# Kernel optimization log

Measured on AMD Instinct MI355X. Metric: run time of the kernel, lower is better.

Reference implementation:

```python
import jax, jax.numpy as jnp
import numpy as np

B, N, S, K, D = 8, 16384, 1024, 32, 64
MLP = [64, 64, 128]
C_IN = 3 + D  # grouped_xyz_norm (3) concat grouped point features (D)
EPS = 1e-5


def setup_inputs() -> dict:
    key = jax.random.key(0)
    ks = jax.random.split(key, 16)
    inp = {
        "xyz": jax.random.normal(ks[0], (B, 3, N), dtype=jnp.float32),
        "points": jax.random.normal(ks[1], (B, D, N), dtype=jnp.float32),
        "sample_idx": jax.random.randint(ks[2], (B, S), 0, N, dtype=jnp.int32),
    }
    last = C_IN
    for i, oc in enumerate(MLP):
        scale = 1.0 / np.sqrt(last)
        inp[f"w{i}"] = jax.random.uniform(ks[3 + 4 * i], (oc, last), jnp.float32, -scale, scale)
        inp[f"b{i}"] = jax.random.uniform(ks[4 + 4 * i], (oc,), jnp.float32, -scale, scale)
        inp[f"g{i}"] = jnp.ones((oc,), jnp.float32)   # BN gamma
        inp[f"be{i}"] = jnp.zeros((oc,), jnp.float32)  # BN beta
        last = oc
    return inp


def _gather(pts, idx):
    # pts: [B,N,C], idx: [B,...] -> [B,...,C]
    return jax.vmap(lambda p, i: p[i])(pts, idx)


def _mlp_layer(x, w, b, g, be):
    # x: [B,C,K,S]; 1x1 Conv2d + BatchNorm2d (training-mode batch stats) + ReLU
    y = jnp.einsum("bcks,oc->boks", x, w) + b[None, :, None, None]
    mu = jnp.mean(y, axis=(0, 2, 3), keepdims=True)
    var = jnp.var(y, axis=(0, 2, 3), keepdims=True)
    y = (y - mu) * jax.lax.rsqrt(var + EPS)
    y = y * g[None, :, None, None] + be[None, :, None, None]
    return jax.nn.relu(y)


def reference(xyz, points, sample_idx, w0, b0, g0, be0, w1, b1, g1, be1, w2, b2, g2, be2):
    xyz_t = jnp.transpose(xyz, (0, 2, 1))      # [B,N,3]
    pts_t = jnp.transpose(points, (0, 2, 1))   # [B,N,D]
    idx_s = sample_idx.astype(jnp.int32)

    new_xyz = _gather(xyz_t, idx_s)            # [B,S,3]

    # square_distance(new_xyz, xyz): [B,S,N]
    d = (jnp.sum(new_xyz ** 2, -1)[:, :, None]
         + jnp.sum(xyz_t ** 2, -1)[:, None, :]
         - 2.0 * jnp.einsum("bsc,bnc->bsn", new_xyz, xyz_t))
    _, idx = jax.lax.top_k(-d, K)              # kNN indices [B,S,K]

    grouped_xyz = _gather(xyz_t, idx)          # [B,S,K,3]
    grouped_norm = grouped_xyz - new_xyz[:, :, None, :]
    grouped_pts = _gather(pts_t, idx)          # [B,S,K,D]
    feat = jnp.concatenate([grouped_norm, grouped_pts], axis=-1)  # [B,S,K,3+D]

    x = jnp.transpose(feat, (0, 3, 2, 1))      # [B,C,K,S]
    x = _mlp_layer(x, w0, b0, g0, be0)
    x = _mlp_layer(x, w1, b1, g1, be1)
    x = _mlp_layer(x, w2, b2, g2, be2)
    new_points = jnp.max(x, axis=2)            # [B,128,S]

    return (jnp.transpose(new_xyz, (0, 2, 1)), new_points, grouped_xyz, idx_s)
```

## Files before the change

### kernel.cpp

```cpp
#include <hip/hip_runtime.h>

constexpr int cB = 8, cN = 16384, cS = 1024, cK = 32, cD = 64;
constexpr int cO2 = 128;
constexpr int PTOT = cB * cS * cK;
constexpr int NBLK = PTOT / 64;
constexpr int C2POS = 128;
constexpr int NBLK2 = PTOT / C2POS;

constexpr int OUT1_OFF = cB * 3 * cS;
constexpr int OUT2_OFF = OUT1_OFF + cB * cO2 * cS;
constexpr int OUT3_OFF = OUT2_OFF + cB * cS * cK * 3;

constexpr size_t WS_PTS  = 0;
constexpr size_t WS_XYZP = WS_PTS  + (size_t)cB * cN * cD * 4;
constexpr size_t WS_IDX  = WS_XYZP + (size_t)cB * cN * 16;
constexpr size_t WS_NORM = WS_IDX  + (size_t)PTOT * 4;
constexpr size_t WS_Y0   = WS_NORM + (size_t)PTOT * 3 * 4;
constexpr size_t WS_Y1   = WS_Y0   + (size_t)PTOT * 64 * 4;
constexpr size_t WS_MX   = WS_Y1   + (size_t)PTOT * 64 * 4;
constexpr size_t WS_MN   = WS_MX   + (size_t)cB * cS * cO2 * 4;
constexpr size_t WS_P0   = WS_MN   + (size_t)cB * cS * cO2 * 4;
constexpr size_t WS_P1   = WS_P0   + (size_t)NBLK * 64 * 2 * 8;
constexpr size_t WS_P2   = WS_P1   + (size_t)NBLK * 64 * 2 * 8;
constexpr size_t WS_BN   = WS_P2   + (size_t)NBLK * 128 * 2 * 8;
constexpr size_t WS_END  = WS_BN   + 3 * 128 * 2 * 4;

__device__ __forceinline__ unsigned keyOf(float d) {
    unsigned u = __float_as_uint(d);
    return u ^ ((unsigned)((int)u >> 31) | 0x80000000u);
}
__device__ __forceinline__ float distNp(float qx, float qy, float qz, float sq, float4 p) {
    float m0 = __fmul_rn(qx, p.x);
    float m1 = __fmul_rn(qy, p.y);
    float m2 = __fmul_rn(qz, p.z);
    float dt = __fadd_rn(__fadd_rn(m0, m1), m2);
    return __fsub_rn(__fadd_rn(sq, p.w), __fmul_rn(2.0f, dt));
}

__global__ __launch_bounds__(256) void k_pack(const float* __restrict__ xyz,
                                              float4* __restrict__ xyzp) {
    int i = blockIdx.x * 256 + threadIdx.x;
    int b = i >> 14, n = i & (cN - 1);
    float x = xyz[(b * 3 + 0) * cN + n];
    float y = xyz[(b * 3 + 1) * cN + n];
    float z = xyz[(b * 3 + 2) * cN + n];
    float sq = __fadd_rn(__fadd_rn(__fmul_rn(x, x), __fmul_rn(y, y)), __fmul_rn(z, z));
    xyzp[i] = make_float4(x, y, z, sq);
}

__global__ __launch_bounds__(256) void k_tr(const float* __restrict__ pts,
                                            float* __restrict__ ptsT) {
    __shared__ float tile[64][65];
    int b = blockIdx.y;
    int n0 = blockIdx.x * 64;
    int tid = threadIdx.x;
    for (int it = 0; it < 16; ++it) {
        int l = it * 256 + tid;
        int c = l >> 6, nn = l & 63;
        tile[nn][c] = pts[((size_t)b * 64 + c) * cN + n0 + nn];
    }
    __syncthreads();
    for (int it = 0; it < 16; ++it) {
        int l = it * 256 + tid;
        int nn = l >> 6, c = l & 63;
        ptsT[((size_t)(b * cN + n0 + nn)) * 64 + c] = tile[nn][c];
    }
}

#define QB 8
#define CAPU 896
#define CAP2 192

__device__ __forceinline__ void selectBin2(const unsigned* __restrict__ h, int lane,
                                           int target, int* Tout, int* cbOut) {
    int base = lane * 8;
    unsigned hh[8];
    unsigned c8 = 0;
#pragma unroll
    for (int i = 0; i < 8; i++) { hh[i] = h[base + i]; c8 += hh[i]; }
    unsigned incl = c8;
#pragma unroll
    for (int off = 1; off < 32; off <<= 1) {
        unsigned t = __shfl_up(incl, (unsigned)off, 32);
        if (lane >= off) incl += t;
    }
    int excl = (int)(incl - c8);
    if (excl < target && target <= (int)incl) {
        int c = excl;
#pragma unroll
        for (int i = 0; i < 8; i++) {
            int nc = c + (int)hh[i];
            if (c < target && target <= nc) { *Tout = base + i; *cbOut = c; }
            c = nc;
        }
    }
}

__global__ __launch_bounds__(256, 4) void k_knn(const float* __restrict__ xyz,
                                                const int* __restrict__ sidx_g,
                                                const float4* __restrict__ xyzp,
                                                int* __restrict__ idxw,
                                                float* __restrict__ normw,
                                                float* __restrict__ outbuf) {
    __shared__ unsigned hist[QB][258];
    __shared__ unsigned short candU[QB][CAPU];
    __shared__ unsigned long long cand2[QB][CAP2];
    __shared__ unsigned cnt[QB], cnt2[QB];
    __shared__ float qxs[QB], qys[QB], qzs[QB], sqs[QB];
    __shared__ int sIdx[QB];
    __shared__ float s1s[QB], tAs[QB], tBs[QB];
    __shared__ int T1s[QB], cb1s[QB], T2s[QB], cb2s[QB];
    __shared__ float fTs[QB];
    __shared__ int ovf[QB], nRf[QB];
    __shared__ int anyR, anyOvfR, anyOvfC;
    __shared__ unsigned order[QB][cK];

    int tid = threadIdx.x;
    int qi = tid >> 5, lane = tid & 31;
    int qbase = blockIdx.x * QB;
    int b = qbase / cS;
    int s0 = qbase % cS;
    const float4* pb = xyzp + (size_t)b * cN;

    if (tid < QB) {
        int si = sidx_g[b * cS + s0 + tid];
        sIdx[tid] = si;
        float x = xyz[(b * 3 + 0) * cN + si];
        float y = xyz[(b * 3 + 1) * cN + si];
        float z = xyz[(b * 3 + 2) * cN + si];
        qxs[tid] = x; qys[tid] = y; qzs[tid] = z;
        sqs[tid] = __fadd_rn(__fadd_rn(__fmul_rn(x, x), __fmul_rn(y, y)), __fmul_rn(z, z));
        cnt[tid] = 0u; cnt2[tid] = 0u;
    }
    if (tid == 0) { anyR = 0; anyOvfR = 0; anyOvfC = 0; }
    for (int i = tid; i < QB * 258; i += 256) ((unsigned*)hist)[i] = 0u;
    __syncthreads();

    float qx = qxs[qi], qy = qys[qi], qz = qzs[qi], qsq = sqs[qi];

    {
        float dmin = 3.4e38f;
        for (int t = 0; t < 64; ++t) {
            float4 p = pb[lane + 32 * t];
            float dot = fmaf(qx, p.x, fmaf(qy, p.y, qz * p.z));
            float d = fmaf(-2.0f, dot, qsq + p.w);
            dmin = fminf(dmin, d);
        }
        float rmax = dmin;
#pragma unroll
        for (int off = 16; off; off >>= 1)
            rmax = fmaxf(rmax, __shfl_xor(rmax, off, 32));
        if (lane == 0) {
            float R = fmaxf(rmax, 1e-12f);
            float s1 = 254.0f / R;
            s1s[qi] = s1;
            tAs[qi] = qsq * s1;
            tBs[qi] = -2.0f * s1;
        }
    }
    __syncthreads();

    float lqx[QB], lqy[QB], lqz[QB], lS[QB], lA[QB], lB[QB];
#pragma unroll
    for (int q = 0; q < QB; q++) {
        lqx[q] = qxs[q]; lqy[q] = qys[q]; lqz[q] = qzs[q];
        lS[q] = s1s[q]; lA[q] = tAs[q]; lB[q] = tBs[q];
    }

    for (int j = 0; j < cN / 256; ++j) {
        int n = j * 256 + tid;
        float4 p = pb[n];
#pragma unroll
        for (int q = 0; q < QB; ++q) {
            float dot = fmaf(lqx[q], p.x, fmaf(lqy[q], p.y, lqz[q] * p.z));
            float t = fmaf(dot, lB[q], fmaf(p.w, lS[q], lA[q]));
            if (t < 258.0f) {
                int bin = __float2int_rz(fmaxf(t, 0.0f));
                atomicAdd(&hist[q][bin], 1u);
                unsigned pos = atomicAdd(&cnt[q], 1u);
                if (pos < CAPU) candU[q][pos] = (unsigned short)n;
            }
        }
    }
    __syncthreads();

    selectBin2(hist[qi], lane, cK, &T1s[qi], &cb1s[qi]);
    __syncthreads();
    if (tid < QB) {
        int T1 = T1s[tid];
        int acc = cb1s[tid] + (int)hist[tid][T1] + (int)hist[tid][T1 + 1];
        int ov = (cnt[tid] > CAPU) ? 1 : 0;
        int nr = (acc > CAP2) ? 1 : 0;
        ovf[tid] = ov; nRf[tid] = nr;
        fTs[tid] = (float)(T1 + 2);
        if (nr) atomicOr(&anyR, 1);
        if (nr && ov) atomicOr(&anyOvfR, 1);
        if (ov) atomicOr(&anyOvfC, 1);
    }
    __syncthreads();

    if (anyR) {
        for (int i = tid; i < QB * 258; i += 256) ((unsigned*)hist)[i] = 0u;
        __syncthreads();
        if (anyOvfR) {
            int lT1[QB], go[QB];
#pragma unroll
            for (int q = 0; q < QB; q++) { lT1[q] = T1s[q]; go[q] = nRf[q] & ovf[q]; }
            for (int j = 0; j < cN / 256; ++j) {
                float4 p = pb[j * 256 + tid];
#pragma unroll
                for (int q = 0; q < QB; ++q) {
                    if (go[q]) {
                        float dot = fmaf(lqx[q], p.x, fmaf(lqy[q], p.y, lqz[q] * p.z));
                        float t = fmaf(dot, lB[q], fmaf(p.w, lS[q], lA[q]));
                        float um = fmaxf(t, 0.0f) - (float)lT1[q];
                        if (um >= 0.0f && um < 2.0f)
                            atomicAdd(&hist[q][min(255, __float2int_rz(um * 128.0f))], 1u);
                    }
                }
            }
        }
        if (nRf[qi] && !ovf[qi]) {
            float fT1 = (float)T1s[qi];
            int m = (int)cnt[qi];
            for (int i = lane; i < m; i += 32) {
                int n = candU[qi][i];
                float4 p = pb[n];
                float dot = fmaf(qx, p.x, fmaf(qy, p.y, qz * p.z));
                float t = fmaf(dot, tBs[qi], fmaf(p.w, s1s[qi], tAs[qi]));
                float um = fmaxf(t, 0.0f) - fT1;
                if (um >= 0.0f && um < 2.0f)
                    atomicAdd(&hist[qi][min(255, __float2int_rz(um * 128.0f))], 1u);
            }
        }
        __syncthreads();
        if (nRf[qi]) selectBin2(hist[qi], lane, cK - cb1s[qi], &T2s[qi], &cb2s[qi]);
        __syncthreads();
        if (tid < QB && nRf[tid])
            fTs[tid] = (float)T1s[tid] + (float)(T2s[tid] + 2) * 0.0078125f;
        __syncthreads();
    }

    if (anyOvfC) {
        float lt[QB]; int go[QB]; float lsq[QB];
#pragma unroll
        for (int q = 0; q < QB; q++) { lt[q] = fTs[q]; go[q] = ovf[q]; lsq[q] = sqs[q]; }
        for (int j = 0; j < cN / 256; ++j) {
            int n = j * 256 + tid;
            float4 p = pb[n];
#pragma unroll
            for (int q = 0; q < QB; ++q) {
                if (go[q]) {
                    float dot = fmaf(lqx[q], p.x, fmaf(lqy[q], p.y, lqz[q] * p.z));
                    float t = fmaf(dot, lB[q], fmaf(p.w, lS[q], lA[q]));
                    if (t < lt[q]) {
                        float de = distNp(lqx[q], lqy[q], lqz[q], lsq[q], p);
                        unsigned pos = atomicAdd(&cnt2[q], 1u);
                        if (pos < CAP2)
                            cand2[q][pos] = ((unsigned long long)keyOf(de) << 32) | (unsigned)n;
                    }
                }
            }
        }
    }
    if (!ovf[qi]) {
        float fT = fTs[qi];
        int m = (int)cnt[qi];
        for (int i = lane; i < m; i += 32) {
            int n = candU[qi][i];
            float4 p = pb[n];
            float dot = fmaf(qx, p.x, fmaf(qy, p.y, qz * p.z));
            float t = fmaf(dot, tBs[qi], fmaf(p.w, s1s[qi], tAs[qi]));
            if (t < fT) {
                float de = distNp(qx, qy, qz, qsq, p);
                unsigned pos = atomicAdd(&cnt2[qi], 1u);
                if (pos < CAP2)
                    cand2[qi][pos] = ((unsigned long long)keyOf(de) << 32) | (unsigned)n;
            }
        }
    }
    __syncthreads();

    int m2 = (int)min(cnt2[qi], (unsigned)CAP2);
    for (int r = 0; r < cK; ++r) {
        unsigned long long best = ~0ull;
        int bslot = -1;
        for (int i = lane; i < m2; i += 32) {
            unsigned long long v = cand2[qi][i];
            if (v < best) { best = v; bslot = i; }
        }
#pragma unroll
        for (int off = 16; off; off >>= 1) {
            unsigned long long ov = __shfl_xor(best, off, 32);
            int os = __shfl_xor(bslot, off, 32);
            if (ov < best) { best = ov; bslot = os; }
        }
        if (lane == 0) {
            order[qi][r] = (best != ~0ull) ? (unsigned)(best & 0xFFFFFFFFull) : 0u;
            if (bslot >= 0) cand2[qi][bslot] = ~0ull;
        }
    }

    {
        int r = lane;
        int s = s0 + qi;
        int n = (int)order[qi][r];
        size_t pos = (size_t)(b * cS + s) * cK + r;
        idxw[pos] = n;
        float px = xyz[(b * 3 + 0) * cN + n];
        float py = xyz[(b * 3 + 1) * cN + n];
        float pz = xyz[(b * 3 + 2) * cN + n];
        outbuf[OUT2_OFF + pos * 3 + 0] = px;
        outbuf[OUT2_OFF + pos * 3 + 1] = py;
        outbuf[OUT2_OFF + pos * 3 + 2] = pz;
        normw[pos * 3 + 0] = __fsub_rn(px, qxs[qi]);
        normw[pos * 3 + 1] = __fsub_rn(py, qys[qi]);
        normw[pos * 3 + 2] = __fsub_rn(pz, qzs[qi]);
        if (r == 0) {
            outbuf[OUT3_OFF + b * cS + s] = (float)sIdx[qi];
            outbuf[(b * 3 + 0) * cS + s] = qxs[qi];
            outbuf[(b * 3 + 1) * cS + s] = qys[qi];
            outbuf[(b * 3 + 2) * cS + s] = qzs[qi];
        }
    }
}

__global__ __launch_bounds__(256) void k_conv0(const int* __restrict__ idxw,
                                               const float* __restrict__ normw,
                                               const float* __restrict__ ptsT,
                                               const float* __restrict__ w0,
                                               const float* __restrict__ b0,
                                               float* __restrict__ y0,
                                               double* __restrict__ part0) {
    __shared__ __align__(16) float fA[64][68];
    __shared__ __align__(16) float wT[68 * 68];
    __shared__ float ps[16][64];
    __shared__ float pq[16][64];
    __shared__ float bl[64];
    int tid = threadIdx.x;
    int blk = blockIdx.x;
    int b = blk >> 9;
    int s0 = (blk & 511) << 1;
    size_t posbase = ((size_t)b * cS + s0) * cK;

    for (int l = tid; l < 64 * 67; l += 256) {
        int o = l / 67, c = l - o * 67;
        wT[c * 68 + o] = w0[l];
    }
    if (tid < 68) wT[67 * 68 + tid] = 0.0f;
    if (tid < 64) bl[tid] = b0[tid];
    {
        int kk = tid >> 2, p = tid & 3;
        size_t pos = posbase + kk;
        int n = idxw[pos];
        const float* pr = ptsT + ((size_t)b * cN + n) * 64 + p * 16;
        float* frow = &fA[kk][3 + p * 16];
#pragma unroll
        for (int q4 = 0; q4 < 4; q4++) {
            float4 v = *(const float4*)(pr + q4 * 4);
            frow[q4 * 4 + 0] = v.x; frow[q4 * 4 + 1] = v.y;
            frow[q4 * 4 + 2] = v.z; frow[q4 * 4 + 3] = v.w;
        }
        if (p == 0) {
            fA[kk][0] = normw[pos * 3 + 0];
            fA[kk][1] = normw[pos * 3 + 1];
            fA[kk][2] = normw[pos * 3 + 2];
            fA[kk][67] = 0.0f;
        }
    }
    __syncthreads();

    int ty = tid >> 4, tx = tid & 15;
    float acc[4][4];
#pragma unroll
    for (int i = 0; i < 4; i++)
#pragma unroll
        for (int j = 0; j < 4; j++) acc[i][j] = bl[tx * 4 + j];

    for (int c4 = 0; c4 < 17; ++c4) {
        float4 wv[4];
#pragma unroll
        for (int cc = 0; cc < 4; cc++)
            wv[cc] = *(const float4*)&wT[(c4 * 4 + cc) * 68 + tx * 4];
#pragma unroll
        for (int i = 0; i < 4; i++) {
            float4 a = *(const float4*)&fA[ty * 4 + i][c4 * 4];
            acc[i][0] = fmaf(a.x, wv[0].x, acc[i][0]);
            acc[i][1] = fmaf(a.x, wv[0].y, acc[i][1]);
            acc[i][2] = fmaf(a.x, wv[0].z, acc[i][2]);
            acc[i][3] = fmaf(a.x, wv[0].w, acc[i][3]);
            acc[i][0] = fmaf(a.y, wv[1].x, acc[i][0]);
            acc[i][1] = fmaf(a.y, wv[1].y, acc[i][1]);
            acc[i][2] = fmaf(a.y, wv[1].z, acc[i][2]);
            acc[i][3] = fmaf(a.y, wv[1].w, acc[i][3]);
            acc[i][0] = fmaf(a.z, wv[2].x, acc[i][0]);
            acc[i][1] = fmaf(a.z, wv[2].y, acc[i][1]);
            acc[i][2] = fmaf(a.z, wv[2].z, acc[i][2]);
            acc[i][3] = fmaf(a.z, wv[2].w, acc[i][3]);
            acc[i][0] = fmaf(a.w, wv[3].x, acc[i][0]);
            acc[i][1] = fmaf(a.w, wv[3].y, acc[i][1]);
            acc[i][2] = fmaf(a.w, wv[3].z, acc[i][2]);
            acc[i][3] = fmaf(a.w, wv[3].w, acc[i][3]);
        }
    }
#pragma unroll
    for (int i = 0; i < 4; i++) {
        int kk = ty * 4 + i;
        float4 o4 = make_float4(acc[i][0], acc[i][1], acc[i][2], acc[i][3]);
        *(float4*)(y0 + (posbase + kk) * 64 + tx * 4) = o4;
    }
#pragma unroll
    for (int j = 0; j < 4; j++) {
        float s = acc[0][j] + acc[1][j] + acc[2][j] + acc[3][j];
        float q = acc[0][j] * acc[0][j] + acc[1][j] * acc[1][j] +
                  acc[2][j] * acc[2][j] + acc[3][j] * acc[3][j];
        ps[ty][tx * 4 + j] = s;
        pq[ty][tx * 4 + j] = q;
    }
    __syncthreads();
    if (tid < 64) {
        float s = 0.f, q = 0.f;
        for (int t = 0; t < 16; t++) { s += ps[t][tid]; q += pq[t][tid]; }
        part0[((size_t)blk * 64 + tid) * 2 + 0] = (double)s;
        part0[((size_t)blk * 64 + tid) * 2 + 1] = (double)q;
    }
}

__global__ __launch_bounds__(256) void k_conv1(const float* __restrict__ yin,
                                               const float2* __restrict__ bnin,
                                               const float* __restrict__ w,
                                               const float* __restrict__ bb,
                                               float* __restrict__ yout,
                                               double* __restrict__ part) {
    __shared__ __align__(16) float fA[64][68];
    __shared__ __align__(16) float wT[64 * 68];
    __shared__ float ps[16][64];
    __shared__ float pq[16][64];
    __shared__ float bl[64], al[64], sl[64];
    int tid = threadIdx.x;
    int blk = blockIdx.x;
    int b = blk >> 9;
    int s0 = (blk & 511) << 1;
    size_t posbase = ((size_t)b * cS + s0) * cK;

    if (tid < 64) {
        bl[tid] = bb[tid];
        float2 t = bnin[tid];
        al[tid] = t.x; sl[tid] = t.y;
    }
    __syncthreads();
    for (int l = tid; l < 64 * 64; l += 256) {
        int o = l >> 6, c = l & 63;
        wT[c * 68 + o] = w[l];
    }
    {
        int kk = tid >> 2, p = tid & 3;
        const float* yr = yin + (posbase + kk) * 64 + p * 16;
#pragma unroll
        for (int q4 = 0; q4 < 4; q4++) {
            float4 v = *(const float4*)(yr + q4 * 4);
            int c = p * 16 + q4 * 4;
            v.x = fmaxf(fmaf(v.x, al[c + 0], sl[c + 0]), 0.0f);
            v.y = fmaxf(fmaf(v.y, al[c + 1], sl[c + 1]), 0.0f);
            v.z = fmaxf(fmaf(v.z, al[c + 2], sl[c + 2]), 0.0f);
            v.w = fmaxf(fmaf(v.w, al[c + 3], sl[c + 3]), 0.0f);
            *(float4*)&fA[kk][c] = v;
        }
    }
    __syncthreads();

    int ty = tid >> 4, tx = tid & 15;
    float acc[4][4];
#pragma unroll
    for (int i = 0; i < 4; i++)
#pragma unroll
        for (int j = 0; j < 4; j++) acc[i][j] = bl[tx * 4 + j];

    for (int c4 = 0; c4 < 16; ++c4) {
        float4 wv[4];
#pragma unroll
        for (int cc = 0; cc < 4; cc++)
            wv[cc] = *(const float4*)&wT[(c4 * 4 + cc) * 68 + tx * 4];
#pragma unroll
        for (int i = 0; i < 4; i++) {
            float4 a = *(const float4*)&fA[ty * 4 + i][c4 * 4];
            acc[i][0] = fmaf(a.x, wv[0].x, acc[i][0]);
            acc[i][1] = fmaf(a.x, wv[0].y, acc[i][1]);
            acc[i][2] = fmaf(a.x, wv[0].z, acc[i][2]);
            acc[i][3] = fmaf(a.x, wv[0].w, acc[i][3]);
            acc[i][0] = fmaf(a.y, wv[1].x, acc[i][0]);
            acc[i][1] = fmaf(a.y, wv[1].y, acc[i][1]);
            acc[i][2] = fmaf(a.y, wv[1].z, acc[i][2]);
            acc[i][3] = fmaf(a.y, wv[1].w, acc[i][3]);
            acc[i][0] = fmaf(a.z, wv[2].x, acc[i][0]);
            acc[i][1] = fmaf(a.z, wv[2].y, acc[i][1]);
            acc[i][2] = fmaf(a.z, wv[2].z, acc[i][2]);
            acc[i][3] = fmaf(a.z, wv[2].w, acc[i][3]);
            acc[i][0] = fmaf(a.w, wv[3].x, acc[i][0]);
            acc[i][1] = fmaf(a.w, wv[3].y, acc[i][1]);
            acc[i][2] = fmaf(a.w, wv[3].z, acc[i][2]);
            acc[i][3] = fmaf(a.w, wv[3].w, acc[i][3]);
        }
    }
#pragma unroll
    for (int i = 0; i < 4; i++) {
        int kk = ty * 4 + i;
        float4 o4 = make_float4(acc[i][0], acc[i][1], acc[i][2], acc[i][3]);
        *(float4*)(yout + (posbase + kk) * 64 + tx * 4) = o4;
    }
#pragma unroll
    for (int j = 0; j < 4; j++) {
        float s = acc[0][j] + acc[1][j] + acc[2][j] + acc[3][j];
        float q = acc[0][j] * acc[0][j] + acc[1][j] * acc[1][j] +
                  acc[2][j] * acc[2][j] + acc[3][j] * acc[3][j];
        ps[ty][tx * 4 + j] = s;
        pq[ty][tx * 4 + j] = q;
    }
    __syncthreads();
    if (tid < 64) {
        float s = 0.f, q = 0.f;
        for (int t = 0; t < 16; t++) { s += ps[t][tid]; q += pq[t][tid]; }
        part[((size_t)blk * 64 + tid) * 2 + 0] = (double)s;
        part[((size_t)blk * 64 + tid) * 2 + 1] = (double)q;
    }
}

__global__ __launch_bounds__(256) void k_conv2(const float* __restrict__ y1,
                                               const float2* __restrict__ bn1,
                                               const float* __restrict__ w2,
                                               const float* __restrict__ b2,
                                               float* __restrict__ mx,
                                               float* __restrict__ mn,
                                               double* __restrict__ part2) {
    __shared__ __align__(16) float fAT[64 * 132];
    __shared__ __align__(16) float wT[64 * 132];
    __shared__ float al[64], sl[64], bl[128];
    int tid = threadIdx.x;
    int blk = blockIdx.x;
    int b = blk >> 8;
    int s0 = (blk & 255) << 2;
    size_t posbase = ((size_t)b * cS + s0) * cK;

    if (tid < 64) { float2 t = bn1[tid]; al[tid] = t.x; sl[tid] = t.y; }
    if (tid < 128) bl[tid] = b2[tid];
    __syncthreads();

    {
        int r = tid >> 1, half = tid & 1;
        const float* yr = y1 + (posbase + r) * 64 + half * 32;
#pragma unroll
        for (int q = 0; q < 8; q++) {
            float4 v = *(const float4*)(yr + q * 4);
            int c = half * 32 + q * 4;
            v.x = fmaxf(fmaf(v.x, al[c + 0], sl[c + 0]), 0.0f);
            v.y = fmaxf(fmaf(v.y, al[c + 1], sl[c + 1]), 0.0f);
            v.z = fmaxf(fmaf(v.z, al[c + 2], sl[c + 2]), 0.0f);
            v.w = fmaxf(fmaf(v.w, al[c + 3], sl[c + 3]), 0.0f);
            fAT[(c + 0) * 132 + r] = v.x;
            fAT[(c + 1) * 132 + r] = v.y;
            fAT[(c + 2) * 132 + r] = v.z;
            fAT[(c + 3) * 132 + r] = v.w;
        }
    }
    for (int l = tid; l < 128 * 64; l += 256) {
        int o = l >> 6, c = l & 63;
        wT[c * 132 + o] = w2[l];
    }
    __syncthreads();

    int ry = tid >> 4, tx = tid & 15;
    float acc[8][8];
#pragma unroll
    for (int i = 0; i < 8; i++) {
#pragma unroll
        for (int j = 0; j < 4; j++) acc[i][j] = bl[tx * 4 + j];
#pragma unroll
        for (int j = 4; j < 8; j++) acc[i][j] = bl[64 + tx * 4 + (j - 4)];
    }

    for (int c = 0; c < 64; ++c) {
        const float* fb = fAT + c * 132;
        const float* wb = wT + c * 132;
        float4 a0 = *(const float4*)(fb + ry * 8);
        float4 a1 = *(const float4*)(fb + ry * 8 + 4);
        float4 w0v = *(const float4*)(wb + tx * 4);
        float4 w1v = *(const float4*)(wb + 64 + tx * 4);
        float av[8] = {a0.x, a0.y, a0.z, a0.w, a1.x, a1.y, a1.z, a1.w};
        float wv[8] = {w0v.x, w0v.y, w0v.z, w0v.w, w1v.x, w1v.y, w1v.z, w1v.w};
#pragma unroll
        for (int i = 0; i < 8; i++)
#pragma unroll
            for (int j = 0; j < 8; j++)
                acc[i][j] = fmaf(av[i], wv[j], acc[i][j]);
    }
    __syncthreads();

    float* ps  = wT;
    float* pq  = wT + 16 * 128;
    float* pmx = wT + 32 * 128;
    float* pmn = wT + 48 * 128;
#pragma unroll
    for (int j = 0; j < 8; j++) {
        int o = (j < 4) ? (tx * 4 + j) : (64 + tx * 4 + (j - 4));
        float s = 0.f, q = 0.f;
        float mv = -3.402823466e+38f, nv = 3.402823466e+38f;
#pragma unroll
        for (int i = 0; i < 8; i++) {
            float v = acc[i][j];
            s += v; q += v * v;
            mv = fmaxf(mv, v); nv = fminf(nv, v);
        }
        ps[ry * 128 + o] = s;
        pq[ry * 128 + o] = q;
        pmx[ry * 128 + o] = mv;
        pmn[ry * 128 + o] = nv;
    }
    __syncthreads();
    if (tid < 128) {
        float s = 0.f, q = 0.f;
        for (int t = 0; t < 16; t++) { s += ps[t * 128 + tid]; q += pq[t * 128 + tid]; }
        part2[((size_t)blk * 128 + tid) * 2 + 0] = (double)s;
        part2[((size_t)blk * 128 + tid) * 2 + 1] = (double)q;
    }
    for (int e = tid; e < 512; e += 256) {
        int sg = e >> 7, o = e & 127;
        float mv = -3.402823466e+38f, nv = 3.402823466e+38f;
        for (int t = sg * 4; t < sg * 4 + 4; ++t) {
            mv = fmaxf(mv, pmx[t * 128 + o]);
            nv = fminf(nv, pmn[t * 128 + o]);
        }
        int s = s0 + sg;
        mx[((size_t)b * cS + s) * 128 + o] = mv;
        mn[((size_t)b * cS + s) * 128 + o] = nv;
    }
}

__global__ __launch_bounds__(256) void k_fin(const double* __restrict__ part, int nblk,
                                             int oc,
                                             const float* __restrict__ g,
                                             const float* __restrict__ be,
                                             float2* __restrict__ bnout) {
    __shared__ double rs[256], rq[256];
    int o = blockIdx.x;
    int tid = threadIdx.x;
    double s = 0.0, q = 0.0;
    for (int i = tid; i < nblk; i += 256) {
        const double* p = part + ((size_t)i * oc + o) * 2;
        s += p[0];
        q += p[1];
    }
    rs[tid] = s; rq[tid] = q;
    __syncthreads();
    for (int off = 128; off; off >>= 1) {
        if (tid < off) { rs[tid] += rs[tid + off]; rq[tid] += rq[tid + off]; }
        __syncthreads();
    }
    if (tid == 0) {
        double cntv = (double)PTOT;
        double mu = rs[0] / cntv;
        double var = rq[0] / cntv - mu * mu;
        if (var < 0.0) var = 0.0;
        float a = (float)((double)g[o] / sqrt(var + 1e-5));
        float sh = (float)((double)be[o] - mu * (double)a);
        bnout[o] = make_float2(a, sh);
    }
}

__global__ __launch_bounds__(256) void k_final(const float* __restrict__ mx,
                                               const float* __restrict__ mn,
                                               const float2* __restrict__ bn2,
                                               float* __restrict__ out1) {
    int i = blockIdx.x * 256 + threadIdx.x;
    int b = i >> 17;
    int r = i & ((1 << 17) - 1);
    int o = r >> 10;
    int s = r & 1023;
    float2 t = bn2[o];
    size_t idx = ((size_t)b * cS + s) * 128 + o;
    float M = (t.x >= 0.0f) ? mx[idx] : mn[idx];
    out1[i] = fmaxf(t.x * M + t.y, 0.0f);
}

extern "C" void kernel_launch(void* const* d_in, const int* in_sizes, int n_in,
                              void* d_out, int out_size, void* d_ws, size_t ws_size,
                              hipStream_t stream) {
    (void)in_sizes; (void)n_in; (void)out_size;
    const float* xyz = (const float*)d_in[0];
    const float* pts = (const float*)d_in[1];
    const int* sidx  = (const int*)d_in[2];
    const float* w0  = (const float*)d_in[3];
    const float* b0  = (const float*)d_in[4];
    const float* g0  = (const float*)d_in[5];
    const float* be0 = (const float*)d_in[6];
    const float* w1  = (const float*)d_in[7];
    const float* b1  = (const float*)d_in[8];
    const float* g1  = (const float*)d_in[9];
    const float* be1 = (const float*)d_in[10];
    const float* w2  = (const float*)d_in[11];
    const float* b2  = (const float*)d_in[12];
    const float* g2  = (const float*)d_in[13];
    const float* be2 = (const float*)d_in[14];
    float* out = (float*)d_out;
    char* ws = (char*)d_ws;
    if (ws_size < WS_END) return;

    float* ptsT  = (float*)(ws + WS_PTS);
    float4* xyzp = (float4*)(ws + WS_XYZP);
    int* idxw    = (int*)(ws + WS_IDX);
    float* normw = (float*)(ws + WS_NORM);
    float* y0    = (float*)(ws + WS_Y0);
    float* y1    = (float*)(ws + WS_Y1);
    float* mx    = (float*)(ws + WS_MX);
    float* mn    = (float*)(ws + WS_MN);
    double* p0   = (double*)(ws + WS_P0);
    double* p1   = (double*)(ws + WS_P1);
    double* p2   = (double*)(ws + WS_P2);
    float2* bnb  = (float2*)(ws + WS_BN);

    hipLaunchKernelGGL(k_pack, dim3(cB * cN / 256), dim3(256), 0, stream, xyz, xyzp);
    hipLaunchKernelGGL(k_tr, dim3(cN / 64, cB), dim3(256), 0, stream, pts, ptsT);
    hipLaunchKernelGGL(k_knn, dim3(cB * cS / QB), dim3(256), 0, stream,
                       xyz, sidx, xyzp, idxw, normw, out);
    hipLaunchKernelGGL(k_conv0, dim3(NBLK), dim3(256), 0, stream,
                       idxw, normw, ptsT, w0, b0, y0, p0);
    hipLaunchKernelGGL(k_fin, dim3(64), dim3(256), 0, stream, p0, NBLK, 64, g0, be0, bnb);
    hipLaunchKernelGGL(k_conv1, dim3(NBLK), dim3(256), 0, stream, y0, bnb, w1, b1, y1, p1);
    hipLaunchKernelGGL(k_fin, dim3(64), dim3(256), 0, stream, p1, NBLK, 64, g1, be1, bnb + 128);
    hipLaunchKernelGGL(k_conv2, dim3(NBLK2), dim3(256), 0, stream,
                       y1, bnb + 128, w2, b2, mx, mn, p2);
    hipLaunchKernelGGL(k_fin, dim3(128), dim3(256), 0, stream, p2, NBLK2, 128, g2, be2, bnb + 256);
    hipLaunchKernelGGL(k_final, dim3(cB * cO2 * cS / 256), dim3(256), 0, stream,
                       mx, mn, bnb + 256, out + OUT1_OFF);
}
```

Baseline: 446.1 us.

## Use ballot bitmasks for kNN candidates, retile conv0/conv1, merge prep kernels

The kNN kernel stops appending candidate indices into a capped shared array through atomics. It now records per-wavefront ballot bitmasks of passing points and rescans those bits in the refine and collect phases, which removes the overflow fallback passes over all N points. conv0 and conv1 now process 128 positions per block with a transposed feature tile and an 8x4 register tile per thread, which halves the block count and raises FMA work per shared load. The pack and transpose kernels are merged into one launch. The bitmask walk is serial per lane and may be uneven across lanes, and the larger register tile raises register pressure.

```diff
diff --git a/kernel.cpp b/kernel.cpp
--- a/kernel.cpp
+++ b/kernel.cpp
@@ -3,9 +3,7 @@
 constexpr int cB = 8, cN = 16384, cS = 1024, cK = 32, cD = 64;
 constexpr int cO2 = 128;
 constexpr int PTOT = cB * cS * cK;
-constexpr int NBLK = PTOT / 64;
-constexpr int C2POS = 128;
-constexpr int NBLK2 = PTOT / C2POS;
+constexpr int NBLK2 = PTOT / 128;
 
 constexpr int OUT1_OFF = cB * 3 * cS;
 constexpr int OUT2_OFF = OUT1_OFF + cB * cO2 * cS;
@@ -20,9 +18,9 @@
 constexpr size_t WS_MX   = WS_Y1   + (size_t)PTOT * 64 * 4;
 constexpr size_t WS_MN   = WS_MX   + (size_t)cB * cS * cO2 * 4;
 constexpr size_t WS_P0   = WS_MN   + (size_t)cB * cS * cO2 * 4;
-constexpr size_t WS_P1   = WS_P0   + (size_t)NBLK * 64 * 2 * 8;
-constexpr size_t WS_P2   = WS_P1   + (size_t)NBLK * 64 * 2 * 8;
-constexpr size_t WS_BN   = WS_P2   + (size_t)NBLK * 128 * 2 * 8;
+constexpr size_t WS_P1   = WS_P0   + (size_t)NBLK2 * 64 * 2 * 8;
+constexpr size_t WS_P2   = WS_P1   + (size_t)NBLK2 * 64 * 2 * 8;
+constexpr size_t WS_BN   = WS_P2   + (size_t)NBLK2 * 128 * 2 * 8;
 constexpr size_t WS_END  = WS_BN   + 3 * 128 * 2 * 4;
 
 __device__ __forceinline__ unsigned keyOf(float d) {
@@ -37,38 +35,39 @@
     return __fsub_rn(__fadd_rn(sq, p.w), __fmul_rn(2.0f, dt));
 }
 
-__global__ __launch_bounds__(256) void k_pack(const float* __restrict__ xyz,
+__global__ __launch_bounds__(256) void k_prep(const float* __restrict__ pts,
+                                              const float* __restrict__ xyz,
+                                              float* __restrict__ ptsT,
                                               float4* __restrict__ xyzp) {
-    int i = blockIdx.x * 256 + threadIdx.x;
-    int b = i >> 14, n = i & (cN - 1);
-    float x = xyz[(b * 3 + 0) * cN + n];
-    float y = xyz[(b * 3 + 1) * cN + n];
-    float z = xyz[(b * 3 + 2) * cN + n];
-    float sq = __fadd_rn(__fadd_rn(__fmul_rn(x, x), __fmul_rn(y, y)), __fmul_rn(z, z));
-    xyzp[i] = make_float4(x, y, z, sq);
-}
-
-__global__ __launch_bounds__(256) void k_tr(const float* __restrict__ pts,
-                                            float* __restrict__ ptsT) {
     __shared__ float tile[64][65];
-    int b = blockIdx.y;
-    int n0 = blockIdx.x * 64;
+    int blk = blockIdx.x;
     int tid = threadIdx.x;
-    for (int it = 0; it < 16; ++it) {
-        int l = it * 256 + tid;
-        int c = l >> 6, nn = l & 63;
-        tile[nn][c] = pts[((size_t)b * 64 + c) * cN + n0 + nn];
-    }
-    __syncthreads();
-    for (int it = 0; it < 16; ++it) {
-        int l = it * 256 + tid;
-        int nn = l >> 6, c = l & 63;
-        ptsT[((size_t)(b * cN + n0 + nn)) * 64 + c] = tile[nn][c];
+    if (blk < 2048) {
+        int b = blk >> 8;
+        int n0 = (blk & 255) * 64;
+        for (int it = 0; it < 16; ++it) {
+            int l = it * 256 + tid;
+            int c = l >> 6, nn = l & 63;
+            tile[nn][c] = pts[((size_t)b * 64 + c) * cN + n0 + nn];
+        }
+        __syncthreads();
+        for (int it = 0; it < 16; ++it) {
+            int l = it * 256 + tid;
+            int nn = l >> 6, c = l & 63;
+            ptsT[((size_t)(b * cN + n0 + nn)) * 64 + c] = tile[nn][c];
+        }
+    } else {
+        int i = (blk - 2048) * 256 + tid;
+        int b = i >> 14, n = i & (cN - 1);
+        float x = xyz[(b * 3 + 0) * cN + n];
+        float y = xyz[(b * 3 + 1) * cN + n];
+        float z = xyz[(b * 3 + 2) * cN + n];
+        float sq = __fadd_rn(__fadd_rn(__fmul_rn(x, x), __fmul_rn(y, y)), __fmul_rn(z, z));
+        xyzp[i] = make_float4(x, y, z, sq);
     }
 }
 
 #define QB 8
-#define CAPU 896
 #define CAP2 192
 
 __device__ __forceinline__ void selectBin2(const unsigned* __restrict__ h, int lane,
@@ -103,20 +102,21 @@
                                                 float* __restrict__ normw,
                                                 float* __restrict__ outbuf) {
     __shared__ unsigned hist[QB][258];
-    __shared__ unsigned short candU[QB][CAPU];
+    __shared__ unsigned long long wmask[QB][256];
     __shared__ unsigned long long cand2[QB][CAP2];
-    __shared__ unsigned cnt[QB], cnt2[QB];
+    __shared__ unsigned cnt2[QB];
     __shared__ float qxs[QB], qys[QB], qzs[QB], sqs[QB];
     __shared__ int sIdx[QB];
     __shared__ float s1s[QB], tAs[QB], tBs[QB];
     __shared__ int T1s[QB], cb1s[QB], T2s[QB], cb2s[QB];
     __shared__ float fTs[QB];
-    __shared__ int ovf[QB], nRf[QB];
-    __shared__ int anyR, anyOvfR, anyOvfC;
+    __shared__ int nRf[QB];
+    __shared__ int anyR;
     __shared__ unsigned order[QB][cK];
 
     int tid = threadIdx.x;
     int qi = tid >> 5, lane = tid & 31;
+    int wid = tid >> 6;
     int qbase = blockIdx.x * QB;
     int b = qbase / cS;
     int s0 = qbase % cS;
@@ -130,9 +130,9 @@
         float z = xyz[(b * 3 + 2) * cN + si];
         qxs[tid] = x; qys[tid] = y; qzs[tid] = z;
         sqs[tid] = __fadd_rn(__fadd_rn(__fmul_rn(x, x), __fmul_rn(y, y)), __fmul_rn(z, z));
-        cnt[tid] = 0u; cnt2[tid] = 0u;
-    }
-    if (tid == 0) { anyR = 0; anyOvfR = 0; anyOvfC = 0; }
+        cnt2[tid] = 0u;
+    }
+    if (tid == 0) anyR = 0;
     for (int i = tid; i < QB * 258; i += 256) ((unsigned*)hist)[i] = 0u;
     __syncthreads();
 
@@ -166,19 +166,19 @@
         lqx[q] = qxs[q]; lqy[q] = qys[q]; lqz[q] = qzs[q];
         lS[q] = s1s[q]; lA[q] = tAs[q]; lB[q] = tBs[q];
     }
+    bool wlead = (tid & 63) == 0;
 
     for (int j = 0; j < cN / 256; ++j) {
-        int n = j * 256 + tid;
-        float4 p = pb[n];
+        float4 p = pb[j * 256 + tid];
 #pragma unroll
         for (int q = 0; q < QB; ++q) {
             float dot = fmaf(lqx[q], p.x, fmaf(lqy[q], p.y, lqz[q] * p.z));
             float t = fmaf(dot, lB[q], fmaf(p.w, lS[q], lA[q]));
+            unsigned long long mk = __ballot(t < 258.0f);
+            if (wlead) wmask[q][j * 4 + wid] = mk;
             if (t < 258.0f) {
                 int bin = __float2int_rz(fmaxf(t, 0.0f));
                 atomicAdd(&hist[q][bin], 1u);
-                unsigned pos = atomicAdd(&cnt[q], 1u);
-                if (pos < CAPU) candU[q][pos] = (unsigned short)n;
             }
         }
     }
@@ -189,48 +189,32 @@
     if (tid < QB) {
         int T1 = T1s[tid];
         int acc = cb1s[tid] + (int)hist[tid][T1] + (int)hist[tid][T1 + 1];
-        int ov = (cnt[tid] > CAPU) ? 1 : 0;
         int nr = (acc > CAP2) ? 1 : 0;
-        ovf[tid] = ov; nRf[tid] = nr;
+        nRf[tid] = nr;
         fTs[tid] = (float)(T1 + 2);
         if (nr) atomicOr(&anyR, 1);
-        if (nr && ov) atomicOr(&anyOvfR, 1);
-        if (ov) atomicOr(&anyOvfC, 1);
     }
     __syncthreads();
 
     if (anyR) {
         for (int i = tid; i < QB * 258; i += 256) ((unsigned*)hist)[i] = 0u;
         __syncthreads();
-        if (anyOvfR) {
-            int lT1[QB], go[QB];
-#pragma unroll
-            for (int q = 0; q < QB; q++) { lT1[q] = T1s[q]; go[q] = nRf[q] & ovf[q]; }
-            for (int j = 0; j < cN / 256; ++j) {
-                float4 p = pb[j * 256 + tid];
-#pragma unroll
-                for (int q = 0; q < QB; ++q) {
-                    if (go[q]) {
-                        float dot = fmaf(lqx[q], p.x, fmaf(lqy[q], p.y, lqz[q] * p.z));
-                        float t = fmaf(dot, lB[q], fmaf(p.w, lS[q], lA[q]));
-                        float um = fmaxf(t, 0.0f) - (float)lT1[q];
-                        if (um >= 0.0f && um < 2.0f)
-                            atomicAdd(&hist[q][min(255, __float2int_rz(um * 128.0f))], 1u);
-                    }
+        if (nRf[qi]) {
+            float fT1 = (float)T1s[qi];
+            float tB = tBs[qi], tS = s1s[qi], tA = tAs[qi];
+            for (int w = lane; w < 256; w += 32) {
+                unsigned long long m = wmask[qi][w];
+                int base = w * 64;
+                while (m) {
+                    int bit = (int)__ffsll((unsigned long long)m) - 1;
+                    m &= m - 1;
+                    float4 p = pb[base + bit];
+                    float dot = fmaf(qx, p.x, fmaf(qy, p.y, qz * p.z));
+                    float t = fmaf(dot, tB, fmaf(p.w, tS, tA));
+                    float um = fmaxf(t, 0.0f) - fT1;
+                    if (um >= 0.0f && um < 2.0f)
+                        atomicAdd(&hist[qi][min(255, __float2int_rz(um * 128.0f))], 1u);
                 }
-            }
-        }
-        if (nRf[qi] && !ovf[qi]) {
-            float fT1 = (float)T1s[qi];
-            int m = (int)cnt[qi];
-            for (int i = lane; i < m; i += 32) {
-                int n = candU[qi][i];
-                float4 p = pb[n];
-                float dot = fmaf(qx, p.x, fmaf(qy, p.y, qz * p.z));
-                float t = fmaf(dot, tBs[qi], fmaf(p.w, s1s[qi], tAs[qi]));
-                float um = fmaxf(t, 0.0f) - fT1;
-                if (um >= 0.0f && um < 2.0f)
-                    atomicAdd(&hist[qi][min(255, __float2int_rz(um * 128.0f))], 1u);
             }
         }
         __syncthreads();
@@ -241,41 +225,25 @@
         __syncthreads();
     }
 
-    if (anyOvfC) {
-        float lt[QB]; int go[QB]; float lsq[QB];
-#pragma unroll
-        for (int q = 0; q < QB; q++) { lt[q] = fTs[q]; go[q] = ovf[q]; lsq[q] = sqs[q]; }
-        for (int j = 0; j < cN / 256; ++j) {
-            int n = j * 256 + tid;
-            float4 p = pb[n];
-#pragma unroll
-            for (int q = 0; q < QB; ++q) {
-                if (go[q]) {
-                    float dot = fmaf(lqx[q], p.x, fmaf(lqy[q], p.y, lqz[q] * p.z));
-                    float t = fmaf(dot, lB[q], fmaf(p.w, lS[q], lA[q]));
-                    if (t < lt[q]) {
-                        float de = distNp(lqx[q], lqy[q], lqz[q], lsq[q], p);
-                        unsigned pos = atomicAdd(&cnt2[q], 1u);
-                        if (pos < CAP2)
-                            cand2[q][pos] = ((unsigned long long)keyOf(de) << 32) | (unsigned)n;
-                    }
+    {
+        float fT = fTs[qi];
+        float tB = tBs[qi], tS = s1s[qi], tA = tAs[qi];
+        for (int w = lane; w < 256; w += 32) {
+            unsigned long long m = wmask[qi][w];
+            int base = w * 64;
+            while (m) {
+                int bit = (int)__ffsll((unsigned long long)m) - 1;
+                m &= m - 1;
+                int n = base + bit;
+                float4 p = pb[n];
+                float dot = fmaf(qx, p.x, fmaf(qy, p.y, qz * p.z));
+                float t = fmaf(dot, tB, fmaf(p.w, tS, tA));
+                if (t < fT) {
+                    float de = distNp(qx, qy, qz, qsq, p);
+                    unsigned pos = atomicAdd(&cnt2[qi], 1u);
+                    if (pos < CAP2)
+                        cand2[qi][pos] = ((unsigned long long)keyOf(de) << 32) | (unsigned)n;
                 }
-            }
-        }
-    }
-    if (!ovf[qi]) {
-        float fT = fTs[qi];
-        int m = (int)cnt[qi];
-        for (int i = lane; i < m; i += 32) {
-            int n = candU[qi][i];
-            float4 p = pb[n];
-            float dot = fmaf(qx, p.x, fmaf(qy, p.y, qz * p.z));
-            float t = fmaf(dot, tBs[qi], fmaf(p.w, s1s[qi], tAs[qi]));
-            if (t < fT) {
-                float de = distNp(qx, qy, qz, qsq, p);
-                unsigned pos = atomicAdd(&cnt2[qi], 1u);
-                if (pos < CAP2)
-                    cand2[qi][pos] = ((unsigned long long)keyOf(de) << 32) | (unsigned)n;
             }
         }
     }
@@ -332,95 +300,84 @@
                                                const float* __restrict__ b0,
                                                float* __restrict__ y0,
                                                double* __restrict__ part0) {
-    __shared__ __align__(16) float fA[64][68];
-    __shared__ __align__(16) float wT[68 * 68];
-    __shared__ float ps[16][64];
-    __shared__ float pq[16][64];
+    __shared__ __align__(16) float fAT[67 * 132];
+    __shared__ __align__(16) float wT[67 * 68];
     __shared__ float bl[64];
     int tid = threadIdx.x;
     int blk = blockIdx.x;
-    int b = blk >> 9;
-    int s0 = (blk & 511) << 1;
+    int b = blk >> 8;
+    int s0 = (blk & 255) << 2;
     size_t posbase = ((size_t)b * cS + s0) * cK;
 
     for (int l = tid; l < 64 * 67; l += 256) {
         int o = l / 67, c = l - o * 67;
         wT[c * 68 + o] = w0[l];
     }
-    if (tid < 68) wT[67 * 68 + tid] = 0.0f;
     if (tid < 64) bl[tid] = b0[tid];
     {
-        int kk = tid >> 2, p = tid & 3;
-        size_t pos = posbase + kk;
+        int r = tid >> 1, half = tid & 1;
+        size_t pos = posbase + r;
         int n = idxw[pos];
-        const float* pr = ptsT + ((size_t)b * cN + n) * 64 + p * 16;
-        float* frow = &fA[kk][3 + p * 16];
-#pragma unroll
-        for (int q4 = 0; q4 < 4; q4++) {
-            float4 v = *(const float4*)(pr + q4 * 4);
-            frow[q4 * 4 + 0] = v.x; frow[q4 * 4 + 1] = v.y;
-            frow[q4 * 4 + 2] = v.z; frow[q4 * 4 + 3] = v.w;
-        }
-        if (p == 0) {
-            fA[kk][0] = normw[pos * 3 + 0];
-            fA[kk][1] = normw[pos * 3 + 1];
-            fA[kk][2] = normw[pos * 3 + 2];
-            fA[kk][67] = 0.0f;
-        }
-    }
-    __syncthreads();
-
-    int ty = tid >> 4, tx = tid & 15;
-    float acc[4][4];
-#pragma unroll
-    for (int i = 0; i < 4; i++)
+        const float* pr = ptsT + ((size_t)b * cN + n) * 64 + half * 32;
+#pragma unroll
+        for (int q = 0; q < 8; q++) {
+            float4 v = *(const float4*)(pr + q * 4);
+            int c = 3 + half * 32 + q * 4;
+            fAT[(c + 0) * 132 + r] = v.x;
+            fAT[(c + 1) * 132 + r] = v.y;
+            fAT[(c + 2) * 132 + r] = v.z;
+            fAT[(c + 3) * 132 + r] = v.w;
+        }
+        if (half == 0) {
+            fAT[0 * 132 + r] = normw[pos * 3 + 0];
+            fAT[1 * 132 + r] = normw[pos * 3 + 1];
+            fAT[2 * 132 + r] = normw[pos * 3 + 2];
+        }
+    }
+    __syncthreads();
+
+    int ry = tid >> 4, tx = tid & 15;
+    float acc[8][4];
+#pragma unroll
+    for (int i = 0; i < 8; i++)
 #pragma unroll
         for (int j = 0; j < 4; j++) acc[i][j] = bl[tx * 4 + j];
 
-    for (int c4 = 0; c4 < 17; ++c4) {
-        float4 wv[4];
-#pragma unroll
-        for (int cc = 0; cc < 4; cc++)
-            wv[cc] = *(const float4*)&wT[(c4 * 4 + cc) * 68 + tx * 4];
-#pragma unroll
-        for (int i = 0; i < 4; i++) {
-            float4 a = *(const float4*)&fA[ty * 4 + i][c4 * 4];
-            acc[i][0] = fmaf(a.x, wv[0].x, acc[i][0]);
-            acc[i][1] = fmaf(a.x, wv[0].y, acc[i][1]);
-            acc[i][2] = fmaf(a.x, wv[0].z, acc[i][2]);
-            acc[i][3] = fmaf(a.x, wv[0].w, acc[i][3]);
-            acc[i][0] = fmaf(a.y, wv[1].x, acc[i][0]);
-            acc[i][1] = fmaf(a.y, wv[1].y, acc[i][1]);
-            acc[i][2] = fmaf(a.y, wv[1].z, acc[i][2]);
-            acc[i][3] = fmaf(a.y, wv[1].w, acc[i][3]);
-            acc[i][0] = fmaf(a.z, wv[2].x, acc[i][0]);
-            acc[i][1] = fmaf(a.z, wv[2].y, acc[i][1]);
-            acc[i][2] = fmaf(a.z, wv[2].z, acc[i][2]);
-            acc[i][3] = fmaf(a.z, wv[2].w, acc[i][3]);
-            acc[i][0] = fmaf(a.w, wv[3].x, acc[i][0]);
-            acc[i][1] = fmaf(a.w, wv[3].y, acc[i][1]);
-            acc[i][2] = fmaf(a.w, wv[3].z, acc[i][2]);
-            acc[i][3] = fmaf(a.w, wv[3].w, acc[i][3]);
-        }
-    }
-#pragma unroll
-    for (int i = 0; i < 4; i++) {
-        int kk = ty * 4 + i;
+    for (int c = 0; c < 67; ++c) {
+        const float* fb = fAT + c * 132;
+        float4 a0 = *(const float4*)(fb + ry * 8);
+        float4 a1 = *(const float4*)(fb + ry * 8 + 4);
+        float4 wv = *(const float4*)&wT[c * 68 + tx * 4];
+        float av[8] = {a0.x, a0.y, a0.z, a0.w, a1.x, a1.y, a1.z, a1.w};
+#pragma unroll
+        for (int i = 0; i < 8; i++) {
+            acc[i][0] = fmaf(av[i], wv.x, acc[i][0]);
+            acc[i][1] = fmaf(av[i], wv.y, acc[i][1]);
+            acc[i][2] = fmaf(av[i], wv.z, acc[i][2]);
+            acc[i][3] = fmaf(av[i], wv.w, acc[i][3]);
+        }
+    }
+#pragma unroll
+    for (int i = 0; i < 8; i++) {
         float4 o4 = make_float4(acc[i][0], acc[i][1], acc[i][2], acc[i][3]);
-        *(float4*)(y0 + (posbase + kk) * 64 + tx * 4) = o4;
-    }
+        *(float4*)(y0 + (posbase + ry * 8 + i) * 64 + tx * 4) = o4;
+    }
+    __syncthreads();
+
+    float* ps = wT;
+    float* pq = wT + 16 * 64;
 #pragma unroll
     for (int j = 0; j < 4; j++) {
-        float s = acc[0][j] + acc[1][j] + acc[2][j] + acc[3][j];
-        float q = acc[0][j] * acc[0][j] + acc[1][j] * acc[1][j] +
-                  acc[2][j] * acc[2][j] + acc[3][j] * acc[3][j];
-        ps[ty][tx * 4 + j] = s;
-        pq[ty][tx * 4 + j] = q;
+        float s = 0.f, q = 0.f;
+#pragma unroll
+        for (int i = 0; i < 8; i++) { float v = acc[i][j]; s += v; q += v * v; }
+        ps[ry * 64 + tx * 4 + j] = s;
+        pq[ry * 64 + tx * 4 + j] = q;
     }
     __syncthreads();
     if (tid < 64) {
         float s = 0.f, q = 0.f;
-        for (int t = 0; t < 16; t++) { s += ps[t][tid]; q += pq[t][tid]; }
+        for (int t = 0; t < 16; t++) { s += ps[t * 64 + tid]; q += pq[t * 64 + tid]; }
         part0[((size_t)blk * 64 + tid) * 2 + 0] = (double)s;
         part0[((size_t)blk * 64 + tid) * 2 + 1] = (double)q;
     }
@@ -432,15 +389,13 @@
                                                const float* __restrict__ bb,
                                                float* __restrict__ yout,
                                                double* __restrict__ part) {
-    __shared__ __align__(16) float fA[64][68];
+    __shared__ __align__(16) float fAT[64 * 132];
     __shared__ __align__(16) float wT[64 * 68];
-    __shared__ float ps[16][64];
-    __shared__ float pq[16][64];
     __shared__ float bl[64], al[64], sl[64];
     int tid = threadIdx.x;
     int blk = blockIdx.x;
-    int b = blk >> 9;
-    int s0 = (blk & 511) << 1;
+    int b = blk >> 8;
+    int s0 = (blk & 255) << 2;
     size_t posbase = ((size_t)b * cS + s0) * cK;
 
     if (tid < 64) {
@@ -454,72 +409,66 @@
         wT[c * 68 + o] = w[l];
     }
     {
-        int kk = tid >> 2, p = tid & 3;
-        const float* yr = yin + (posbase + kk) * 64 + p * 16;
-#pragma unroll
-        for (int q4 = 0; q4 < 4; q4++) {
-            float4 v = *(const float4*)(yr + q4 * 4);
-            int c = p * 16 + q4 * 4;
+        int r = tid >> 1, half = tid & 1;
+        const float* yr = yin + (posbase + r) * 64 + half * 32;
+#pragma unroll
+        for (int q = 0; q < 8; q++) {
+            float4 v = *(const float4*)(yr + q * 4);
+            int c = half * 32 + q * 4;
             v.x = fmaxf(fmaf(v.x, al[c + 0], sl[c + 0]), 0.0f);
             v.y = fmaxf(fmaf(v.y, al[c + 1], sl[c + 1]), 0.0f);
             v.z = fmaxf(fmaf(v.z, al[c + 2], sl[c + 2]), 0.0f);
             v.w = fmaxf(fmaf(v.w, al[c + 3], sl[c + 3]), 0.0f);
-            *(float4*)&fA[kk][c] = v;
-        }
-    }
-    __syncthreads();
-
-    int ty = tid >> 4, tx = tid & 15;
-    float acc[4][4];
-#pragma unroll
-    for (int i = 0; i < 4; i++)
+            fAT[(c + 0) * 132 + r] = v.x;
+            fAT[(c + 1) * 132 + r] = v.y;
+            fAT[(c + 2) * 132 + r] = v.z;
+            fAT[(c + 3) * 132 + r] = v.w;
+        }
+    }
+    __syncthreads();
+
+    int ry = tid >> 4, tx = tid & 15;
+    float acc[8][4];
+#pragma unroll
+    for (int i = 0; i < 8; i++)
 #pragma unroll
         for (int j = 0; j < 4; j++) acc[i][j] = bl[tx * 4 + j];
 
-    for (int c4 = 0; c4 < 16; ++c4) {
-        float4 wv[4];
-#pragma unroll
-        for (int cc = 0; cc < 4; cc++)
-            wv[cc] = *(const float4*)&wT[(c4 * 4 + cc) * 68 + tx * 4];
-#pragma unroll
-        for (int i = 0; i < 4; i++) {
-            float4 a = *(const float4*)&fA[ty * 4 + i][c4 * 4];
-            acc[i][0] = fmaf(a.x, wv[0].x, acc[i][0]);
-            acc[i][1] = fmaf(a.x, wv[0].y, acc[i][1]);
-            acc[i][2] = fmaf(a.x, wv[0].z, acc[i][2]);
-            acc[i][3] = fmaf(a.x, wv[0].w, acc[i][3]);
-            acc[i][0] = fmaf(a.y, wv[1].x, acc[i][0]);
-            acc[i][1] = fmaf(a.y, wv[1].y, acc[i][1]);
-            acc[i][2] = fmaf(a.y, wv[1].z, acc[i][2]);
-            acc[i][3] = fmaf(a.y, wv[1].w, acc[i][3]);
-            acc[i][0] = fmaf(a.z, wv[2].x, acc[i][0]);
-            acc[i][1] = fmaf(a.z, wv[2].y, acc[i][1]);
-            acc[i][2] = fmaf(a.z, wv[2].z, acc[i][2]);
-            acc[i][3] = fmaf(a.z, wv[2].w, acc[i][3]);
-            acc[i][0] = fmaf(a.w, wv[3].x, acc[i][0]);
-            acc[i][1] = fmaf(a.w, wv[3].y, acc[i][1]);
-            acc[i][2] = fmaf(a.w, wv[3].z, acc[i][2]);
-            acc[i][3] = fmaf(a.w, wv[3].w, acc[i][3]);
-        }
-    }
-#pragma unroll
-    for (int i = 0; i < 4; i++) {
-        int kk = ty * 4 + i;
+    for (int c = 0; c < 64; ++c) {
+        const float* fb = fAT + c * 132;
+        float4 a0 = *(const float4*)(fb + ry * 8);
+        float4 a1 = *(const float4*)(fb + ry * 8 + 4);
+        float4 wv = *(const float4*)&wT[c * 68 + tx * 4];
+        float av[8] = {a0.x, a0.y, a0.z, a0.w, a1.x, a1.y, a1.z, a1.w};
+#pragma unroll
+        for (int i = 0; i < 8; i++) {
+            acc[i][0] = fmaf(av[i], wv.x, acc[i][0]);
+            acc[i][1] = fmaf(av[i], wv.y, acc[i][1]);
+            acc[i][2] = fmaf(av[i], wv.z, acc[i][2]);
+            acc[i][3] = fmaf(av[i], wv.w, acc[i][3]);
+        }
+    }
+#pragma unroll
+    for (int i = 0; i < 8; i++) {
         float4 o4 = make_float4(acc[i][0], acc[i][1], acc[i][2], acc[i][3]);
-        *(float4*)(yout + (posbase + kk) * 64 + tx * 4) = o4;
-    }
+        *(float4*)(yout + (posbase + ry * 8 + i) * 64 + tx * 4) = o4;
+    }
+    __syncthreads();
+
+    float* ps = wT;
+    float* pq = wT + 16 * 64;
 #pragma unroll
     for (int j = 0; j < 4; j++) {
-        float s = acc[0][j] + acc[1][j] + acc[2][j] + acc[3][j];
-        float q = acc[0][j] * acc[0][j] + acc[1][j] * acc[1][j] +
-                  acc[2][j] * acc[2][j] + acc[3][j] * acc[3][j];
-        ps[ty][tx * 4 + j] = s;
-        pq[ty][tx * 4 + j] = q;
+        float s = 0.f, q = 0.f;
+#pragma unroll
+        for (int i = 0; i < 8; i++) { float v = acc[i][j]; s += v; q += v * v; }
+        ps[ry * 64 + tx * 4 + j] = s;
+        pq[ry * 64 + tx * 4 + j] = q;
     }
     __syncthreads();
     if (tid < 64) {
         float s = 0.f, q = 0.f;
-        for (int t = 0; t < 16; t++) { s += ps[t][tid]; q += pq[t][tid]; }
+        for (int t = 0; t < 16; t++) { s += ps[t * 64 + tid]; q += pq[t * 64 + tid]; }
         part[((size_t)blk * 64 + tid) * 2 + 0] = (double)s;
         part[((size_t)blk * 64 + tid) * 2 + 1] = (double)q;
     }
@@ -717,15 +666,15 @@
     double* p2   = (double*)(ws + WS_P2);
     float2* bnb  = (float2*)(ws + WS_BN);
 
-    hipLaunchKernelGGL(k_pack, dim3(cB * cN / 256), dim3(256), 0, stream, xyz, xyzp);
-    hipLaunchKernelGGL(k_tr, dim3(cN / 64, cB), dim3(256), 0, stream, pts, ptsT);
+    hipLaunchKernelGGL(k_prep, dim3(2048 + cB * cN / 256), dim3(256), 0, stream,
+                       pts, xyz, ptsT, xyzp);
     hipLaunchKernelGGL(k_knn, dim3(cB * cS / QB), dim3(256), 0, stream,
                        xyz, sidx, xyzp, idxw, normw, out);
-    hipLaunchKernelGGL(k_conv0, dim3(NBLK), dim3(256), 0, stream,
+    hipLaunchKernelGGL(k_conv0, dim3(NBLK2), dim3(256), 0, stream,
                        idxw, normw, ptsT, w0, b0, y0, p0);
-    hipLaunchKernelGGL(k_fin, dim3(64), dim3(256), 0, stream, p0, NBLK, 64, g0, be0, bnb);
-    hipLaunchKernelGGL(k_conv1, dim3(NBLK), dim3(256), 0, stream, y0, bnb, w1, b1, y1, p1);
-    hipLaunchKernelGGL(k_fin, dim3(64), dim3(256), 0, stream, p1, NBLK, 64, g1, be1, bnb + 128);
+    hipLaunchKernelGGL(k_fin, dim3(64), dim3(256), 0, stream, p0, NBLK2, 64, g0, be0, bnb);
+    hipLaunchKernelGGL(k_conv1, dim3(NBLK2), dim3(256), 0, stream, y0, bnb, w1, b1, y1, p1);
+    hipLaunchKernelGGL(k_fin, dim3(64), dim3(256), 0, stream, p1, NBLK2, 64, g1, be1, bnb + 128);
     hipLaunchKernelGGL(k_conv2, dim3(NBLK2), dim3(256), 0, stream,
                        y1, bnb + 128, w2, b2, mx, mn, p2);
     hipLaunchKernelGGL(k_fin, dim3(128), dim3(256), 0, stream, p2, NBLK2, 128, g2, be2, bnb + 256);
```

After: 395.9 us. 1.13x faster.
